# Kernel tuning notes

Measured on AMD Instinct MI355X. Metric: run time of the kernel, lower is better.

Reference implementation:

```python
import jax, jax.numpy as jnp
import numpy as np

B, S, D, H = 2, 2048, 768, 12
Dh = D // H  # attention_head_size = 64
NEG = -1e9


def setup_inputs() -> dict:
    key = jax.random.key(0)
    ks = jax.random.split(key, 10)
    scale = 1.0 / np.sqrt(D).astype(np.float32)
    inp = {
        "hidden_states": jax.random.normal(ks[0], (B, S, D), jnp.float32),
        "Wq": jax.random.normal(ks[1], (D, D), jnp.float32) * scale,
        "bq": jnp.zeros((D,), jnp.float32),
        "Wk": jax.random.normal(ks[2], (D, D), jnp.float32) * scale,
        "bk": jnp.zeros((D,), jnp.float32),
        "Wv": jax.random.normal(ks[3], (D, D), jnp.float32) * scale,
        "bv": jnp.zeros((D,), jnp.float32),
        "Wo": jax.random.normal(ks[4], (D, D), jnp.float32) * scale,
        "bo": jnp.zeros((D,), jnp.float32),
        "mask": jax.random.randint(ks[5], (B, S), 0, 2).astype(bool),
    }
    return inp


def _heads(x):
    # [B,S,D] -> [B,H,S,Dh]
    return x.reshape(B, S, H, Dh).transpose(0, 2, 1, 3)


def reference(hidden_states, Wq, bq, Wk, bk, Wv, bv, Wo, bo, mask):
    q = _heads(hidden_states @ Wq + bq)
    k = _heads(hidden_states @ Wk + bk)
    v = _heads(hidden_states @ Wv + bv)

    # [B,H,S,S] raw scores
    scores = jnp.einsum("bhqd,bhkd->bhqk", q, k) / np.sqrt(Dh).astype(np.float32)

    # pairwise fg mask: [B,1,S,S]; True where both query and key tokens are fg
    am = mask[:, None, :, None] & mask[:, None, None, :]

    # fg softmax: bg pairs masked to -1e9; bg softmax: fg pairs masked to -1e9
    fg_probs = jax.nn.softmax(jnp.where(am, scores, NEG), axis=-1)
    bg_probs = jnp.where(am, NEG, scores)
    bg_probs = jax.nn.softmax(bg_probs, axis=-1)

    # stitch: take fg probs at fg pairs, bg probs elsewhere (replaces boolean scatter)
    probs = jnp.where(am, fg_probs, bg_probs)

    ctx = jnp.einsum("bhqk,bhkd->bhqd", probs, v)
    ctx = ctx.transpose(0, 2, 1, 3).reshape(B, S, D)
    return ctx @ Wo + bo
```

## Files before the change

kernel.cpp:

```cpp
#include <hip/hip_runtime.h>

typedef float f32x4 __attribute__((ext_vector_type(4)));
typedef short bf16x8 __attribute__((ext_vector_type(8)));

#define MFMA16(a, b, c) __builtin_amdgcn_mfma_f32_16x16x32_bf16((a), (b), (c), 0, 0, 0)

constexpr int S_ = 2048;
constexpr int D_ = 768;
constexpr int H_ = 12;
constexpr int DH = 64;
constexpr int B_ = 2;
constexpr int M_ = B_ * S_;
constexpr int BH = B_ * H_;

typedef unsigned short u16;
typedef unsigned int u32;

__device__ __forceinline__ u16 f2bf(float f) {
  u32 u = __builtin_bit_cast(u32, f);
  u += 0x7fffu + ((u >> 16) & 1u);
  return (u16)(u >> 16);
}
__device__ __forceinline__ u32 pack2(float a, float b) {
  return (u32)f2bf(a) | ((u32)f2bf(b) << 16);
}
__device__ __forceinline__ u32 pack2r(float lo, float hi) {
  u32 a = __builtin_bit_cast(u32, lo) + 0x8000u;
  u32 b = __builtin_bit_cast(u32, hi) + 0x8000u;
  return __builtin_amdgcn_perm(b, a, 0x07060302u);
}

__device__ __forceinline__ void gload16(const void* g, void* l) {
  __builtin_amdgcn_global_load_lds((const __attribute__((address_space(1))) u32*)g,
                                   (__attribute__((address_space(3))) u32*)l, 16, 0, 0);
}

__global__ __launch_bounds__(256) void conv_bf16(const float* __restrict__ in,
                                                 u16* __restrict__ out) {
  int i = blockIdx.x * 256 + threadIdx.x;
  float4 v = ((const float4*)in)[i];
  uint2 r;
  r.x = pack2(v.x, v.y);
  r.y = pack2(v.z, v.w);
  ((uint2*)out)[i] = r;
}

__global__ __launch_bounds__(256) void conv_wT4(const float* __restrict__ Wq,
                                                const float* __restrict__ Wk,
                                                const float* __restrict__ Wv,
                                                const float* __restrict__ Wo,
                                                u16* __restrict__ wqkv,
                                                u16* __restrict__ wo) {
  __shared__ float t[32][33];
  int z = blockIdx.z;
  const float* w = z == 0 ? Wq : z == 1 ? Wk : z == 2 ? Wv : Wo;
  u16* wt = z == 3 ? wo : wqkv + (size_t)z * D_ * D_;
  int k0 = blockIdx.x << 5, n0 = blockIdx.y << 5;
  int x = threadIdx.x & 31, y = threadIdx.x >> 5;
#pragma unroll
  for (int j = 0; j < 4; ++j) t[y + 8 * j][x] = w[(size_t)(k0 + y + 8 * j) * D_ + n0 + x];
  __syncthreads();
#pragma unroll
  for (int j = 0; j < 4; ++j) wt[(size_t)(n0 + y + 8 * j) * D_ + k0 + x] = f2bf(t[x][y + 8 * j]);
}

__global__ __launch_bounds__(256) void canon_mask(const void* __restrict__ mraw,
                                                  float* __restrict__ fm,
                                                  u32* __restrict__ mw) {
  __shared__ int isBool;
  int tid = threadIdx.x;
  if (tid == 0) isBool = 0;
  __syncthreads();
  const int* mi = (const int*)mraw;
  int v = mi[tid];
  if (v != 0 && v != 1) atomicOr(&isBool, 1);
  __syncthreads();
  const unsigned char* mb = (const unsigned char*)mraw;
  int p = blockIdx.x * 256 + tid;
  int m0, m1;
  if (isBool) { m0 = mb[2 * p]; m1 = mb[2 * p + 1]; }
  else        { m0 = mi[2 * p]; m1 = mi[2 * p + 1]; }
  fm[2 * p] = (float)m0;
  fm[2 * p + 1] = (float)m1;
  mw[p] = (m0 ? 0xFFFFu : 0u) | (m1 ? 0xFFFF0000u : 0u);
}

template <int MODE>
__global__ __launch_bounds__(256, 2) void gemm128(const u16* __restrict__ A,
                                                  const u16* __restrict__ Wt,
                                                  const float* __restrict__ bq,
                                                  const float* __restrict__ bk,
                                                  const float* __restrict__ bv,
                                                  u16* __restrict__ oq,
                                                  u16* __restrict__ ok,
                                                  u16* __restrict__ ov,
                                                  float* __restrict__ of,
                                                  float qscale) {
  constexpr int NT = D_ / 64;
  __shared__ __align__(16) u16 lA[2][128 * 64];
  __shared__ __align__(16) u16 lB[2][128 * 64];
  const int tid = threadIdx.x, w = tid >> 6, lane = tid & 63;
  const int g = lane >> 4, c = lane & 15;
  const int m0 = blockIdx.x * 128, n0 = blockIdx.y * 128;
  const int wr = w >> 1, wc = w & 1;
  const int srow = lane >> 3, scb = ((lane & 7) * 16) ^ (srow << 4);
  const int sw = (c & 7) << 4;
  const char* Ab = (const char*)A + (size_t)m0 * (D_ * 2);
  const char* Bb = (const char*)Wt + (size_t)n0 * (D_ * 2);

  auto stage = [&](int buf, int t) {
    int k0b = t * 128;
#pragma unroll
    for (int a = 0; a < 4; ++a) {
      int rr = w * 32 + a * 8;
      gload16(Ab + (size_t)(rr + srow) * (D_ * 2) + k0b + scb, &lA[buf][rr * 64]);
      gload16(Bb + (size_t)(rr + srow) * (D_ * 2) + k0b + scb, &lB[buf][rr * 64]);
    }
  };

  f32x4 acc[4][4] = {};
  auto compute = [&](int buf) {
    const char* pa = (const char*)&lA[buf][0];
    const char* pb = (const char*)&lB[buf][0];
#pragma unroll
    for (int kk = 0; kk < 2; ++kk) {
      const int cs = (kk * 64 + g * 16) ^ sw;
      bf16x8 af[4], bf[4];
#pragma unroll
      for (int i = 0; i < 4; ++i)
        af[i] = *(const bf16x8*)(pa + (wr * 64 + i * 16 + c) * 128 + cs);
#pragma unroll
      for (int j = 0; j < 4; ++j)
        bf[j] = *(const bf16x8*)(pb + (wc * 64 + j * 16 + c) * 128 + cs);
      __builtin_amdgcn_s_setprio(1);
#pragma unroll
      for (int i = 0; i < 4; ++i)
#pragma unroll
        for (int j = 0; j < 4; ++j) acc[i][j] = MFMA16(af[i], bf[j], acc[i][j]);
      __builtin_amdgcn_s_setprio(0);
    }
  };

  stage(0, 0);
  __syncthreads();
  int buf = 0;
#pragma unroll 1
  for (int t = 0; t < NT; ++t) {
    if (t + 1 < NT) stage(buf ^ 1, t + 1);
    compute(buf);
    __syncthreads();
    buf ^= 1;
  }

  if (MODE == 0) {
    const int p = n0 / D_;
    const int nn0 = n0 - p * D_;
    const float* bias = p == 0 ? bq : p == 1 ? bk : bv;
    const float sc = p == 0 ? qscale : 1.0f;
#pragma unroll
    for (int j = 0; j < 4; ++j) {
      int nn = nn0 + wc * 64 + j * 16 + c;
      float bvv = bias[nn];
      int h = nn >> 6, d = nn & 63;
#pragma unroll
      for (int i = 0; i < 4; ++i) {
        int m = m0 + wr * 64 + i * 16 + g * 4;
        int b = m >> 11, s = m & (S_ - 1);
        if (p < 2) {
          u16* dst = (p == 0 ? oq : ok) + ((size_t)(b * H_ + h) * S_ + s) * DH + d;
#pragma unroll
          for (int r = 0; r < 4; ++r) dst[(size_t)r * DH] = f2bf((acc[i][j][r] + bvv) * sc);
        } else {
          int chunk = s >> 5, kq = (s >> 2) & 7;
          int sb = kq < 4 ? 8 * kq : 8 * (kq - 4) + 4;
          uint2 pk;
          pk.x = pack2r(acc[i][j][0] + bvv, acc[i][j][1] + bvv);
          pk.y = pack2r(acc[i][j][2] + bvv, acc[i][j][3] + bvv);
          *(uint2*)(ov + ((size_t)((b * H_ + h) * DH + d)) * S_ + chunk * 32 + sb) = pk;
        }
      }
    }
  } else {
#pragma unroll
    for (int j = 0; j < 4; ++j) {
      int n = n0 + wc * 64 + j * 16 + c;
      float bvv = bq[n];
#pragma unroll
      for (int i = 0; i < 4; ++i) {
        int m = m0 + wr * 64 + i * 16 + g * 4;
#pragma unroll
        for (int r = 0; r < 4; ++r) of[(size_t)(m + r) * D_ + n] = acc[i][j][r] + bvv;
      }
    }
  }
}

__global__ __launch_bounds__(128, 2) void attn(const u16* __restrict__ Q,
                                               const u16* __restrict__ K,
                                               const u16* __restrict__ Vt,
                                               const float* __restrict__ fm,
                                               const u32* __restrict__ mw,
                                               u16* __restrict__ ctx) {
  constexpr int NT = S_ / 64;
  __shared__ __align__(16) u16 lK[2][64 * 64];
  __shared__ __align__(16) u16 lV[2][64 * 64];
  __shared__ __align__(16) u32 lM[S_ / 2];

  const int tid = threadIdx.x;
  const int w = tid >> 6, lane = tid & 63;
  const int g = lane >> 4, c = lane & 15;
  const int bid = blockIdx.x;
  const int wg = (bid & 7) * 96 + (bid >> 3);
  const int qt = wg & 31, bh = wg >> 5;
  const int b = bh / H_, h = bh % H_;
  const int qbase = qt * 64 + w * 32;

  const u16* Qp = Q + ((size_t)bh * S_ + qbase) * DH;
  const char* Kp = (const char*)(K + (size_t)bh * S_ * DH);
  const char* Vp = (const char*)(Vt + (size_t)bh * DH * S_);
  const float* fmp = fm + b * S_;
  const char* mwp = (const char*)(mw + b * (S_ / 2));

  bf16x8 qf[2][2];
#pragma unroll
  for (int qs = 0; qs < 2; ++qs)
#pragma unroll
    for (int kk = 0; kk < 2; ++kk)
      qf[qs][kk] = *(const bf16x8*)(Qp + (qs * 16 + c) * DH + kk * 32 + g * 8);

  u32 ow = (c == 0) ? 0x3F803F80u : 0u;
  uint4 owv = {ow, ow, ow, ow};
  bf16x8 onesf = __builtin_bit_cast(bf16x8, owv);

  const int srow = lane >> 3;
  const int scb = ((lane & 7) * 16) ^ (srow << 4);
  const int sw = (c & 7) << 4;

  f32x4 accf[2][4] = {}, accb[2][4] = {}, alf[2] = {}, alb[2] = {};

  auto stage = [&](int buf, int t) {
    const char* kb_ = Kp + (size_t)t * 8192;
    const char* vb_ = Vp + (size_t)t * 128;
#pragma unroll
    for (int a = 0; a < 4; ++a) {
      int rr = w * 32 + a * 8;
      gload16(kb_ + (size_t)(rr + srow) * 128 + scb, &lK[buf][rr * 64]);
      gload16(vb_ + (size_t)(rr + srow) * 4096 + scb, &lV[buf][rr * 64]);
    }
  };

  auto compute = [&](int buf, int t) {
    const char* kt = (const char*)&lK[buf][0];
    const char* vtl = (const char*)&lV[buf][0];
#pragma unroll
    for (int kc = 0; kc < 2; ++kc) {
      uint2 m01 = *(const uint2*)((const char*)lM + t * 128 + kc * 64 + g * 8);
      uint2 m23 = *(const uint2*)((const char*)lM + t * 128 + kc * 64 + 32 + g * 8);
      bf16x8 k00 = *(const bf16x8*)(kt + (kc * 32 + c) * 128 + ((g * 16) ^ sw));
      bf16x8 k01 = *(const bf16x8*)(kt + (kc * 32 + c) * 128 + ((64 + g * 16) ^ sw));
      bf16x8 k10 = *(const bf16x8*)(kt + (kc * 32 + 16 + c) * 128 + ((g * 16) ^ sw));
      bf16x8 k11 = *(const bf16x8*)(kt + (kc * 32 + 16 + c) * 128 + ((64 + g * 16) ^ sw));
      const int csel = (kc * 64 + g * 16) ^ sw;
      bf16x8 vf0 = *(const bf16x8*)(vtl + (0 * 16 + c) * 128 + csel);
      bf16x8 vf1 = *(const bf16x8*)(vtl + (1 * 16 + c) * 128 + csel);
      bf16x8 vf2 = *(const bf16x8*)(vtl + (2 * 16 + c) * 128 + csel);
      bf16x8 vf3 = *(const bf16x8*)(vtl + (3 * 16 + c) * 128 + csel);
#pragma unroll
      for (int qs = 0; qs < 2; ++qs) {
        f32x4 st0 = {}, st1 = {};
        __builtin_amdgcn_s_setprio(1);
        st0 = MFMA16(k00, qf[qs][0], st0);
        st0 = MFMA16(k01, qf[qs][1], st0);
        st1 = MFMA16(k10, qf[qs][0], st1);
        st1 = MFMA16(k11, qf[qs][1], st1);
        __builtin_amdgcn_s_setprio(0);
        u32 ew0 = pack2r(__builtin_amdgcn_exp2f(st0[0]), __builtin_amdgcn_exp2f(st0[1]));
        u32 ew1 = pack2r(__builtin_amdgcn_exp2f(st0[2]), __builtin_amdgcn_exp2f(st0[3]));
        u32 ew2 = pack2r(__builtin_amdgcn_exp2f(st1[0]), __builtin_amdgcn_exp2f(st1[1]));
        u32 ew3 = pack2r(__builtin_amdgcn_exp2f(st1[2]), __builtin_amdgcn_exp2f(st1[3]));
        u32 pf0 = ew0 & m01.x, pf1 = ew1 & m01.y;
        u32 pf2 = ew2 & m23.x, pf3 = ew3 & m23.y;
        uint4 pfv = {pf0, pf1, pf2, pf3};
        uint4 pbv = {ew0 ^ pf0, ew1 ^ pf1, ew2 ^ pf2, ew3 ^ pf3};
        bf16x8 paf = __builtin_bit_cast(bf16x8, pfv);
        bf16x8 pab = __builtin_bit_cast(bf16x8, pbv);
        __builtin_amdgcn_s_setprio(1);
        accf[qs][0] = MFMA16(paf, vf0, accf[qs][0]);
        accb[qs][0] = MFMA16(pab, vf0, accb[qs][0]);
        accf[qs][1] = MFMA16(paf, vf1, accf[qs][1]);
        accb[qs][1] = MFMA16(pab, vf1, accb[qs][1]);
        accf[qs][2] = MFMA16(paf, vf2, accf[qs][2]);
        accb[qs][2] = MFMA16(pab, vf2, accb[qs][2]);
        accf[qs][3] = MFMA16(paf, vf3, accf[qs][3]);
        accb[qs][3] = MFMA16(pab, vf3, accb[qs][3]);
        alf[qs] = MFMA16(paf, onesf, alf[qs]);
        alb[qs] = MFMA16(pab, onesf, alb[qs]);
        __builtin_amdgcn_s_setprio(0);
      }
    }
  };

  gload16(mwp + w * 2048 + lane * 16, &lM[w * 512]);
  gload16(mwp + w * 2048 + 1024 + lane * 16, &lM[w * 512 + 256]);
  stage(0, 0);
  __syncthreads();

  int buf = 0;
#pragma unroll 1
  for (int t = 0; t < NT; ++t) {
    if (t + 1 < NT) stage(buf ^ 1, t + 1);
    compute(buf, t);
    __syncthreads();
    buf ^= 1;
  }

#pragma unroll
  for (int qs = 0; qs < 2; ++qs) {
    const int qw = qbase + qs * 16;
#pragma unroll
    for (int r = 0; r < 4; ++r) {
      int ql = g * 4 + r;
      float lfr = __shfl(alf[qs][r], g * 16);
      float lbr = __shfl(alb[qs][r], g * 16);
      bool fg = fmp[qw + ql] > 0.5f;
      float inv_f = (lfr > 0.f) ? 1.f / lfr : 0.f;
      float inv_b = (lbr > 0.f) ? 1.f / lbr : 0.f;
      float inv_all = 1.f / (lfr + lbr);
#pragma unroll
      for (int n = 0; n < 4; ++n) {
        float o = fg ? (accf[qs][n][r] * inv_f + accb[qs][n][r] * inv_b)
                     : ((accf[qs][n][r] + accb[qs][n][r]) * inv_all);
        ctx[((size_t)(b * S_ + qw + ql)) * D_ + h * DH + n * 16 + c] = f2bf(o);
      }
    }
  }
}

extern "C" void kernel_launch(void* const* d_in, const int* in_sizes, int n_in,
                              void* d_out, int out_size, void* d_ws, size_t ws_size,
                              hipStream_t stream) {
  const float* hs = (const float*)d_in[0];
  const float* Wq = (const float*)d_in[1];
  const float* bq = (const float*)d_in[2];
  const float* Wk = (const float*)d_in[3];
  const float* bk = (const float*)d_in[4];
  const float* Wv = (const float*)d_in[5];
  const float* bv = (const float*)d_in[6];
  const float* Wo = (const float*)d_in[7];
  const float* bo = (const float*)d_in[8];
  const void* mraw = d_in[9];

  char* ws = (char*)d_ws;
  size_t off = 0;
  auto alloc = [&](size_t bytes) {
    void* p = ws + off;
    off += (bytes + 255) & ~(size_t)255;
    return p;
  };
  u16* hsb = (u16*)alloc((size_t)M_ * D_ * 2);
  u16* wqkvT = (u16*)alloc((size_t)3 * D_ * D_ * 2);
  u16* woT = (u16*)alloc((size_t)D_ * D_ * 2);
  u16* qb = (u16*)alloc((size_t)M_ * D_ * 2);
  u16* kb = (u16*)alloc((size_t)M_ * D_ * 2);
  u16* vtb = (u16*)alloc((size_t)M_ * D_ * 2);
  u16* ctx = (u16*)alloc((size_t)M_ * D_ * 2);
  float* fmf = (float*)alloc((size_t)B_ * S_ * 4);
  u32* mwb = (u32*)alloc((size_t)B_ * S_ / 2 * 4);

  conv_bf16<<<(M_ * D_ / 4 + 255) / 256, 256, 0, stream>>>(hs, hsb);
  conv_wT4<<<dim3(D_ / 32, D_ / 32, 4), 256, 0, stream>>>(Wq, Wk, Wv, Wo, wqkvT, woT);
  canon_mask<<<B_ * S_ / 512, 256, 0, stream>>>(mraw, fmf, mwb);

  const float qscale = 0.125f * 1.44269504088896f;
  gemm128<0><<<dim3(M_ / 128, 3 * D_ / 128), 256, 0, stream>>>(
      hsb, wqkvT, bq, bk, bv, qb, kb, vtb, nullptr, qscale);

  attn<<<dim3(768), 128, 0, stream>>>(qb, kb, vtb, fmf, mwb, ctx);

  gemm128<1><<<dim3(M_ / 128, D_ / 128), 256, 0, stream>>>(
      ctx, woT, bo, nullptr, nullptr, nullptr, nullptr, nullptr, (float*)d_out, 1.0f);
}
```

Measured before the change: 115.8 us.

## Split attention key tiles across four waves with LDS reduction of partial accumulators

```diff
diff --git a/kernel.cpp b/kernel.cpp
--- a/kernel.cpp
+++ b/kernel.cpp
@@ -195,25 +195,27 @@
   }
 }
 
-__global__ __launch_bounds__(128, 2) void attn(const u16* __restrict__ Q,
+__global__ __launch_bounds__(256, 3) void attn(const u16* __restrict__ Q,
                                                const u16* __restrict__ K,
                                                const u16* __restrict__ Vt,
                                                const float* __restrict__ fm,
                                                const u32* __restrict__ mw,
                                                u16* __restrict__ ctx) {
   constexpr int NT = S_ / 64;
-  __shared__ __align__(16) u16 lK[2][64 * 64];
-  __shared__ __align__(16) u16 lV[2][64 * 64];
-  __shared__ __align__(16) u32 lM[S_ / 2];
+  __shared__ __align__(16) char smem[40960];
+  char* lKb = smem;
+  char* lVb = smem + 16384;
+  char* lMb = smem + 32768;
 
   const int tid = threadIdx.x;
   const int w = tid >> 6, lane = tid & 63;
   const int g = lane >> 4, c = lane & 15;
+  const int qh = w & 1, kh = w >> 1;
   const int bid = blockIdx.x;
   const int wg = (bid & 7) * 96 + (bid >> 3);
   const int qt = wg & 31, bh = wg >> 5;
   const int b = bh / H_, h = bh % H_;
-  const int qbase = qt * 64 + w * 32;
+  const int qbase = qt * 64 + qh * 32;
 
   const u16* Qp = Q + ((size_t)bh * S_ + qbase) * DH;
   const char* Kp = (const char*)(K + (size_t)bh * S_ * DH);
@@ -235,73 +237,70 @@
   const int srow = lane >> 3;
   const int scb = ((lane & 7) * 16) ^ (srow << 4);
   const int sw = (c & 7) << 4;
+  const int r8a = w * 2, r8b = w * 2 + 1;
+  const int rowA = r8a * 8 + srow, rowB = r8b * 8 + srow;
 
   f32x4 accf[2][4] = {}, accb[2][4] = {}, alf[2] = {}, alb[2] = {};
 
   auto stage = [&](int buf, int t) {
     const char* kb_ = Kp + (size_t)t * 8192;
     const char* vb_ = Vp + (size_t)t * 128;
-#pragma unroll
-    for (int a = 0; a < 4; ++a) {
-      int rr = w * 32 + a * 8;
-      gload16(kb_ + (size_t)(rr + srow) * 128 + scb, &lK[buf][rr * 64]);
-      gload16(vb_ + (size_t)(rr + srow) * 4096 + scb, &lV[buf][rr * 64]);
-    }
+    gload16(kb_ + (size_t)rowA * 128 + scb, lKb + buf * 8192 + r8a * 1024);
+    gload16(kb_ + (size_t)rowB * 128 + scb, lKb + buf * 8192 + r8b * 1024);
+    gload16(vb_ + (size_t)rowA * 4096 + scb, lVb + buf * 8192 + r8a * 1024);
+    gload16(vb_ + (size_t)rowB * 4096 + scb, lVb + buf * 8192 + r8b * 1024);
   };
 
   auto compute = [&](int buf, int t) {
-    const char* kt = (const char*)&lK[buf][0];
-    const char* vtl = (const char*)&lV[buf][0];
-#pragma unroll
-    for (int kc = 0; kc < 2; ++kc) {
-      uint2 m01 = *(const uint2*)((const char*)lM + t * 128 + kc * 64 + g * 8);
-      uint2 m23 = *(const uint2*)((const char*)lM + t * 128 + kc * 64 + 32 + g * 8);
-      bf16x8 k00 = *(const bf16x8*)(kt + (kc * 32 + c) * 128 + ((g * 16) ^ sw));
-      bf16x8 k01 = *(const bf16x8*)(kt + (kc * 32 + c) * 128 + ((64 + g * 16) ^ sw));
-      bf16x8 k10 = *(const bf16x8*)(kt + (kc * 32 + 16 + c) * 128 + ((g * 16) ^ sw));
-      bf16x8 k11 = *(const bf16x8*)(kt + (kc * 32 + 16 + c) * 128 + ((64 + g * 16) ^ sw));
-      const int csel = (kc * 64 + g * 16) ^ sw;
-      bf16x8 vf0 = *(const bf16x8*)(vtl + (0 * 16 + c) * 128 + csel);
-      bf16x8 vf1 = *(const bf16x8*)(vtl + (1 * 16 + c) * 128 + csel);
-      bf16x8 vf2 = *(const bf16x8*)(vtl + (2 * 16 + c) * 128 + csel);
-      bf16x8 vf3 = *(const bf16x8*)(vtl + (3 * 16 + c) * 128 + csel);
-#pragma unroll
-      for (int qs = 0; qs < 2; ++qs) {
-        f32x4 st0 = {}, st1 = {};
-        __builtin_amdgcn_s_setprio(1);
-        st0 = MFMA16(k00, qf[qs][0], st0);
-        st0 = MFMA16(k01, qf[qs][1], st0);
-        st1 = MFMA16(k10, qf[qs][0], st1);
-        st1 = MFMA16(k11, qf[qs][1], st1);
-        __builtin_amdgcn_s_setprio(0);
-        u32 ew0 = pack2r(__builtin_amdgcn_exp2f(st0[0]), __builtin_amdgcn_exp2f(st0[1]));
-        u32 ew1 = pack2r(__builtin_amdgcn_exp2f(st0[2]), __builtin_amdgcn_exp2f(st0[3]));
-        u32 ew2 = pack2r(__builtin_amdgcn_exp2f(st1[0]), __builtin_amdgcn_exp2f(st1[1]));
-        u32 ew3 = pack2r(__builtin_amdgcn_exp2f(st1[2]), __builtin_amdgcn_exp2f(st1[3]));
-        u32 pf0 = ew0 & m01.x, pf1 = ew1 & m01.y;
-        u32 pf2 = ew2 & m23.x, pf3 = ew3 & m23.y;
-        uint4 pfv = {pf0, pf1, pf2, pf3};
-        uint4 pbv = {ew0 ^ pf0, ew1 ^ pf1, ew2 ^ pf2, ew3 ^ pf3};
-        bf16x8 paf = __builtin_bit_cast(bf16x8, pfv);
-        bf16x8 pab = __builtin_bit_cast(bf16x8, pbv);
-        __builtin_amdgcn_s_setprio(1);
-        accf[qs][0] = MFMA16(paf, vf0, accf[qs][0]);
-        accb[qs][0] = MFMA16(pab, vf0, accb[qs][0]);
-        accf[qs][1] = MFMA16(paf, vf1, accf[qs][1]);
-        accb[qs][1] = MFMA16(pab, vf1, accb[qs][1]);
-        accf[qs][2] = MFMA16(paf, vf2, accf[qs][2]);
-        accb[qs][2] = MFMA16(pab, vf2, accb[qs][2]);
-        accf[qs][3] = MFMA16(paf, vf3, accf[qs][3]);
-        accb[qs][3] = MFMA16(pab, vf3, accb[qs][3]);
-        alf[qs] = MFMA16(paf, onesf, alf[qs]);
-        alb[qs] = MFMA16(pab, onesf, alb[qs]);
-        __builtin_amdgcn_s_setprio(0);
-      }
+    const char* kt = lKb + buf * 8192;
+    const char* vtl = lVb + buf * 8192;
+    const int kc = kh;
+    uint2 m01 = *(const uint2*)(lMb + t * 128 + kc * 64 + g * 8);
+    uint2 m23 = *(const uint2*)(lMb + t * 128 + kc * 64 + 32 + g * 8);
+    bf16x8 k00 = *(const bf16x8*)(kt + (kc * 32 + c) * 128 + ((g * 16) ^ sw));
+    bf16x8 k01 = *(const bf16x8*)(kt + (kc * 32 + c) * 128 + ((64 + g * 16) ^ sw));
+    bf16x8 k10 = *(const bf16x8*)(kt + (kc * 32 + 16 + c) * 128 + ((g * 16) ^ sw));
+    bf16x8 k11 = *(const bf16x8*)(kt + (kc * 32 + 16 + c) * 128 + ((64 + g * 16) ^ sw));
+    const int csel = (kc * 64 + g * 16) ^ sw;
+    bf16x8 vf0 = *(const bf16x8*)(vtl + (0 * 16 + c) * 128 + csel);
+    bf16x8 vf1 = *(const bf16x8*)(vtl + (1 * 16 + c) * 128 + csel);
+    bf16x8 vf2 = *(const bf16x8*)(vtl + (2 * 16 + c) * 128 + csel);
+    bf16x8 vf3 = *(const bf16x8*)(vtl + (3 * 16 + c) * 128 + csel);
+#pragma unroll
+    for (int qs = 0; qs < 2; ++qs) {
+      f32x4 st0 = {}, st1 = {};
+      __builtin_amdgcn_s_setprio(1);
+      st0 = MFMA16(k00, qf[qs][0], st0);
+      st0 = MFMA16(k01, qf[qs][1], st0);
+      st1 = MFMA16(k10, qf[qs][0], st1);
+      st1 = MFMA16(k11, qf[qs][1], st1);
+      __builtin_amdgcn_s_setprio(0);
+      u32 ew0 = pack2r(__builtin_amdgcn_exp2f(st0[0]), __builtin_amdgcn_exp2f(st0[1]));
+      u32 ew1 = pack2r(__builtin_amdgcn_exp2f(st0[2]), __builtin_amdgcn_exp2f(st0[3]));
+      u32 ew2 = pack2r(__builtin_amdgcn_exp2f(st1[0]), __builtin_amdgcn_exp2f(st1[1]));
+      u32 ew3 = pack2r(__builtin_amdgcn_exp2f(st1[2]), __builtin_amdgcn_exp2f(st1[3]));
+      u32 pf0 = ew0 & m01.x, pf1 = ew1 & m01.y;
+      u32 pf2 = ew2 & m23.x, pf3 = ew3 & m23.y;
+      uint4 pfv = {pf0, pf1, pf2, pf3};
+      uint4 pbv = {ew0 ^ pf0, ew1 ^ pf1, ew2 ^ pf2, ew3 ^ pf3};
+      bf16x8 paf = __builtin_bit_cast(bf16x8, pfv);
+      bf16x8 pab = __builtin_bit_cast(bf16x8, pbv);
+      __builtin_amdgcn_s_setprio(1);
+      accf[qs][0] = MFMA16(paf, vf0, accf[qs][0]);
+      accb[qs][0] = MFMA16(pab, vf0, accb[qs][0]);
+      accf[qs][1] = MFMA16(paf, vf1, accf[qs][1]);
+      accb[qs][1] = MFMA16(pab, vf1, accb[qs][1]);
+      accf[qs][2] = MFMA16(paf, vf2, accf[qs][2]);
+      accb[qs][2] = MFMA16(pab, vf2, accb[qs][2]);
+      accf[qs][3] = MFMA16(paf, vf3, accf[qs][3]);
+      accb[qs][3] = MFMA16(pab, vf3, accb[qs][3]);
+      alf[qs] = MFMA16(paf, onesf, alf[qs]);
+      alb[qs] = MFMA16(pab, onesf, alb[qs]);
+      __builtin_amdgcn_s_setprio(0);
     }
   };
 
-  gload16(mwp + w * 2048 + lane * 16, &lM[w * 512]);
-  gload16(mwp + w * 2048 + 1024 + lane * 16, &lM[w * 512 + 256]);
+  gload16(mwp + w * 1024 + lane * 16, lMb + w * 1024);
   stage(0, 0);
   __syncthreads();
 
@@ -314,23 +313,52 @@
     buf ^= 1;
   }
 
-#pragma unroll
-  for (int qs = 0; qs < 2; ++qs) {
-    const int qw = qbase + qs * 16;
-#pragma unroll
-    for (int r = 0; r < 4; ++r) {
-      int ql = g * 4 + r;
-      float lfr = __shfl(alf[qs][r], g * 16);
-      float lbr = __shfl(alb[qs][r], g * 16);
-      bool fg = fmp[qw + ql] > 0.5f;
-      float inv_f = (lfr > 0.f) ? 1.f / lfr : 0.f;
-      float inv_b = (lbr > 0.f) ? 1.f / lbr : 0.f;
-      float inv_all = 1.f / (lfr + lbr);
+  f32x4* red = (f32x4*)smem + (size_t)qh * 1280;
+  if (kh == 1) {
+#pragma unroll
+    for (int qs = 0; qs < 2; ++qs)
 #pragma unroll
       for (int n = 0; n < 4; ++n) {
-        float o = fg ? (accf[qs][n][r] * inv_f + accb[qs][n][r] * inv_b)
-                     : ((accf[qs][n][r] + accb[qs][n][r]) * inv_all);
-        ctx[((size_t)(b * S_ + qw + ql)) * D_ + h * DH + n * 16 + c] = f2bf(o);
+        red[(qs * 4 + n) * 64 + lane] = accf[qs][n];
+        red[(8 + qs * 4 + n) * 64 + lane] = accb[qs][n];
+      }
+    red[16 * 64 + lane] = alf[0];
+    red[17 * 64 + lane] = alf[1];
+    red[18 * 64 + lane] = alb[0];
+    red[19 * 64 + lane] = alb[1];
+  }
+  __syncthreads();
+  if (kh == 0) {
+#pragma unroll
+    for (int qs = 0; qs < 2; ++qs)
+#pragma unroll
+      for (int n = 0; n < 4; ++n) {
+        accf[qs][n] += red[(qs * 4 + n) * 64 + lane];
+        accb[qs][n] += red[(8 + qs * 4 + n) * 64 + lane];
+      }
+    alf[0] += red[16 * 64 + lane];
+    alf[1] += red[17 * 64 + lane];
+    alb[0] += red[18 * 64 + lane];
+    alb[1] += red[19 * 64 + lane];
+
+#pragma unroll
+    for (int qs = 0; qs < 2; ++qs) {
+      const int qw = qbase + qs * 16;
+#pragma unroll
+      for (int r = 0; r < 4; ++r) {
+        int ql = g * 4 + r;
+        float lfr = __shfl(alf[qs][r], g * 16);
+        float lbr = __shfl(alb[qs][r], g * 16);
+        bool fg = fmp[qw + ql] > 0.5f;
+        float inv_f = (lfr > 0.f) ? 1.f / lfr : 0.f;
+        float inv_b = (lbr > 0.f) ? 1.f / lbr : 0.f;
+        float inv_all = 1.f / (lfr + lbr);
+#pragma unroll
+        for (int n = 0; n < 4; ++n) {
+          float o = fg ? (accf[qs][n][r] * inv_f + accb[qs][n][r] * inv_b)
+                       : ((accf[qs][n][r] + accb[qs][n][r]) * inv_all);
+          ctx[((size_t)(b * S_ + qw + ql)) * D_ + h * DH + n * 16 + c] = f2bf(o);
+        }
       }
     }
   }
@@ -375,7 +403,7 @@
   gemm128<0><<<dim3(M_ / 128, 3 * D_ / 128), 256, 0, stream>>>(
       hsb, wqkvT, bq, bk, bv, qb, kb, vtb, nullptr, qscale);
 
-  attn<<<dim3(768), 128, 0, stream>>>(qb, kb, vtb, fmf, mwb, ctx);
+  attn<<<dim3(768), 256, 0, stream>>>(qb, kb, vtb, fmf, mwb, ctx);
 
   gemm128<1><<<dim3(M_ / 128, D_ / 128), 256, 0, stream>>>(
       ctx, woT, bo, nullptr, nullptr, nullptr, nullptr, nullptr, (float*)d_out, 1.0f);
```

Result: faster. 104.7 us (-9.5%).
